# Optimization experiments

Measured on AMD Instinct MI355X. Metric: run time of the kernel, lower is better.

Reference implementation:

```python
import jax, jax.numpy as jnp
import numpy as np

ALPHA = 1.5      # entmax alpha (q parameter)
N_ITER = 50      # entmax-bisect iterations (entmax library default)
B, S, DM, H, HKV, HD = 1, 2048, 2048, 16, 4, 128
ROPE_THETA = 10000.0


def _entmax_p(x):
    """alpha-entmax along last axis via bisection on tau (matches entmax.EntmaxBisect)."""
    am1 = ALPHA - 1.0
    pw = 1.0 / am1
    X = x * am1
    d = x.shape[-1]
    max_val = jnp.max(X, axis=-1, keepdims=True)
    tau_lo = max_val - 1.0                      # _gp(1, alpha) = 1
    tau_hi = max_val - (1.0 / d) ** am1          # _gp(1/d, alpha)
    dm0 = tau_hi - tau_lo

    def body(i, carry):
        tau_lo, dm, tau_m = carry
        dm = dm * 0.5
        tau_m = tau_lo + dm
        p = jnp.maximum(X - tau_m, 0.0) ** pw
        f = jnp.sum(p, axis=-1, keepdims=True) - 1.0
        tau_lo = jnp.where(f >= 0, tau_m, tau_lo)
        return (tau_lo, dm, tau_m)

    tau_lo, dm, tau_m = jax.lax.fori_loop(0, N_ITER, body, (tau_lo, dm0, tau_lo))
    p = jnp.maximum(X - tau_m, 0.0) ** pw
    return p / jnp.sum(p, axis=-1, keepdims=True)  # ensure_sum_one


@jax.custom_vjp
def entmax_bisect(x):
    return _entmax_p(x)

def _emx_fwd(x):
    p = _entmax_p(x)
    return p, p

def _emx_bwd(p, g):
    # entmax library backward: gppr = p^(2-alpha) on support
    gppr = jnp.where(p > 0, p ** (2.0 - ALPHA), 0.0)
    dX = g * gppr
    q = jnp.sum(dX, axis=-1, keepdims=True) / jnp.sum(gppr, axis=-1, keepdims=True)
    return ((dX - q * gppr),)

entmax_bisect.defvjp(_emx_fwd, _emx_bwd)


def _rotate_half(x):
    x1, x2 = x[..., : HD // 2], x[..., HD // 2:]
    return jnp.concatenate([-x2, x1], axis=-1)


def setup_inputs() -> dict:
    key = jax.random.key(0)
    k1, k2, k3, k4, k5 = jax.random.split(key, 5)
    hidden_states = jax.random.normal(k1, (B, S, DM), dtype=jnp.float32)
    wq = jax.random.normal(k2, (H * HD, DM), dtype=jnp.float32) * 0.02
    wk = jax.random.normal(k3, (HKV * HD, DM), dtype=jnp.float32) * 0.02
    wv = jax.random.normal(k4, (HKV * HD, DM), dtype=jnp.float32) * 0.02
    wo = jax.random.normal(k5, (DM, H * HD), dtype=jnp.float32) * 0.02
    # real Llama RoPE position embeddings
    inv_freq = 1.0 / (ROPE_THETA ** (np.arange(0, HD, 2, dtype=np.float32) / HD))
    pos = np.arange(S, dtype=np.float32)
    freqs = pos[:, None] * inv_freq[None, :]          # [S, HD/2]
    emb = np.concatenate([freqs, freqs], axis=-1)     # [S, HD]
    cos = jnp.asarray(np.cos(emb))[None]              # [1, S, HD]
    sin = jnp.asarray(np.sin(emb))[None]
    return {"hidden_states": hidden_states, "cos": cos, "sin": sin,
            "wq": wq, "wk": wk, "wv": wv, "wo": wo}


def reference(hidden_states, cos, sin, wq, wk, wv, wo):
    b, s, _ = hidden_states.shape
    scaling = HD ** -0.5
    # QKV projections -> [B, H, S, HD]
    q = (hidden_states @ wq.T).reshape(b, s, H, HD).transpose(0, 2, 1, 3)
    k = (hidden_states @ wk.T).reshape(b, s, HKV, HD).transpose(0, 2, 1, 3)
    v = (hidden_states @ wv.T).reshape(b, s, HKV, HD).transpose(0, 2, 1, 3)
    # RoPE (cos/sin broadcast over head axis)
    c, sn = cos[:, None, :, :], sin[:, None, :, :]
    q = q * c + _rotate_half(q) * sn
    k = k * c + _rotate_half(k) * sn
    # GQA: repeat kv heads
    g = H // HKV
    k = jnp.repeat(k, g, axis=1)
    v = jnp.repeat(v, g, axis=1)
    scores = jnp.einsum('bhqd,bhkd->bhqk', q, k) * scaling
    causal = jnp.tril(jnp.ones((s, s), dtype=bool))
    scores = jnp.where(causal, scores, -jnp.inf)
    attn = entmax_bisect(scores)                      # [B, H, S, S]
    out = jnp.einsum('bhqk,bhkd->bhqd', attn, v)
    out = out.transpose(0, 2, 1, 3).reshape(b, s, H * HD)
    out = out @ wo.T
    return (out, attn)
```

## Files before the change

### kernel.cpp

```cpp
#include <hip/hip_runtime.h>

typedef __bf16 bf16;
typedef __bf16 bf16x4 __attribute__((ext_vector_type(4)));
typedef __bf16 bf16x8 __attribute__((ext_vector_type(8)));
typedef float f32x4 __attribute__((ext_vector_type(4)));
typedef float f32x2 __attribute__((ext_vector_type(2)));
typedef _Float16 f16x2 __attribute__((ext_vector_type(2)));

#define S 2048
#define DM 2048
#define HD 128
#define H 16
#define NQKV 3072
#define NEWTON_ITERS 12
#define BROW 556
#define MASKV -30000.0f

__device__ __forceinline__ void gl2lds16(const void* g, void* l) {
    __builtin_amdgcn_global_load_lds(
        (const __attribute__((address_space(1))) void*)g,
        (__attribute__((address_space(3))) void*)l, 16, 0, 0);
}

__device__ __forceinline__ void nt_store4(f32x4 v, float* p) {
    __builtin_nontemporal_store(v, (f32x4*)p);
}

template <int CTRL, int RM>
__device__ __forceinline__ float dpp_zero(float x) {
    return __builtin_bit_cast(float, __builtin_amdgcn_update_dpp(
        0, __builtin_bit_cast(int, x), CTRL, RM, 0xf, false));
}
template <int CTRL, int RM>
__device__ __forceinline__ float dpp_self(float x) {
    int xi = __builtin_bit_cast(int, x);
    return __builtin_bit_cast(float, __builtin_amdgcn_update_dpp(xi, xi, CTRL, RM, 0xf, false));
}
__device__ __forceinline__ float wave_bcast63(float x) {
    return __builtin_bit_cast(float, __builtin_amdgcn_readlane(__builtin_bit_cast(int, x), 63));
}
__device__ __forceinline__ float wave_sum(float x) {
    x += dpp_zero<0x111, 0xf>(x);
    x += dpp_zero<0x112, 0xf>(x);
    x += dpp_zero<0x114, 0xf>(x);
    x += dpp_zero<0x118, 0xf>(x);
    x += dpp_zero<0x142, 0xa>(x);
    x += dpp_zero<0x143, 0xc>(x);
    return wave_bcast63(x);
}
__device__ __forceinline__ float wave_fmax(float x) {
    x = fmaxf(x, dpp_self<0x111, 0xf>(x));
    x = fmaxf(x, dpp_self<0x112, 0xf>(x));
    x = fmaxf(x, dpp_self<0x114, 0xf>(x));
    x = fmaxf(x, dpp_self<0x118, 0xf>(x));
    x = fmaxf(x, dpp_self<0x142, 0xa>(x));
    x = fmaxf(x, dpp_self<0x143, 0xc>(x));
    return wave_bcast63(x);
}

__global__ void cvt_all(const float* __restrict__ hid, const float* __restrict__ wq,
                        const float* __restrict__ wk, const float* __restrict__ wv,
                        const float* __restrict__ wo, bf16* __restrict__ bh,
                        bf16* __restrict__ bqkv, bf16* __restrict__ bwo) {
    int i = blockIdx.x * blockDim.x + threadIdx.x;
    const float* src;
    bf16* dst;
    int off;
    if (i < 1048576) { src = hid; dst = bh; off = i; }
    else if (i < 2097152) { src = wq; dst = bqkv; off = i - 1048576; }
    else if (i < 2359296) { src = wk; dst = bqkv + 2048 * 2048; off = i - 2097152; }
    else if (i < 2621440) { src = wv; dst = bqkv + 2048 * 2048 + 512 * 2048; off = i - 2359296; }
    else { src = wo; dst = bwo; off = i - 2621440; }
    float4 f = ((const float4*)src)[off];
    bf16x4 o;
    o[0] = (bf16)f.x; o[1] = (bf16)f.y; o[2] = (bf16)f.z; o[3] = (bf16)f.w;
    ((bf16x4*)dst)[off] = o;
}

template <int BM, int BN>
__global__ __launch_bounds__(256) void gemm_bt(const bf16* __restrict__ A,
                                               const bf16* __restrict__ B,
                                               float* __restrict__ C, int Ndim, int K) {
    __shared__ bf16 As[BM * 32];
    __shared__ bf16 Bs[BN * 32];
    int m0 = blockIdx.x * BM, n0 = blockIdx.y * BN;
    int t = threadIdx.x;
    int l = t & 63, w = t >> 6;
    int lane16 = l & 15, quad = l >> 4;

    const bf16* Abase = A + (size_t)m0 * K;
    const bf16* Bbase = B + (size_t)n0 * K;

    constexpr int MI = BM / 32, NI = BN / 32;
    int wm = (w & 1) * (BM / 2), wn = (w >> 1) * (BN / 2);
    f32x4 acc[MI][NI];
#pragma unroll
    for (int i = 0; i < MI; i++)
#pragma unroll
        for (int j = 0; j < NI; j++) acc[i][j] = (f32x4){0.f, 0.f, 0.f, 0.f};

    constexpr int AG = BM * 4;
    constexpr int BG = BN * 4;

    for (int k0 = 0; k0 < K; k0 += 32) {
#pragma unroll
        for (int it = 0; it < AG / 256; it++) {
            int c = it * 256 + t;
            gl2lds16(Abase + (size_t)(c >> 2) * K + k0 + (c & 3) * 8, &As[(c - l) * 8]);
        }
#pragma unroll
        for (int it = 0; it < BG / 256; it++) {
            int c = it * 256 + t;
            gl2lds16(Bbase + (size_t)(c >> 2) * K + k0 + (c & 3) * 8, &Bs[(c - l) * 8]);
        }
        __syncthreads();
        bf16x8 af[MI], bfr[NI];
#pragma unroll
        for (int i = 0; i < MI; i++)
            af[i] = *(const bf16x8*)&As[(wm + i * 16 + lane16) * 32 + quad * 8];
#pragma unroll
        for (int j = 0; j < NI; j++)
            bfr[j] = *(const bf16x8*)&Bs[(wn + j * 16 + lane16) * 32 + quad * 8];
#pragma unroll
        for (int i = 0; i < MI; i++)
#pragma unroll
            for (int j = 0; j < NI; j++)
                acc[i][j] = __builtin_amdgcn_mfma_f32_16x16x32_bf16(af[i], bfr[j], acc[i][j], 0, 0, 0);
        __syncthreads();
    }
#pragma unroll
    for (int i = 0; i < MI; i++)
#pragma unroll
        for (int j = 0; j < NI; j++) {
            float* cp = C + (size_t)(m0 + wm + i * 16 + quad * 4) * Ndim + n0 + wn + j * 16 + lane16;
#pragma unroll
            for (int r = 0; r < 4; r++) cp[(size_t)r * Ndim] = acc[i][j][r];
        }
}

__global__ void rope_qk(const float* __restrict__ qkv, const float* __restrict__ cosb,
                        const float* __restrict__ sinb, bf16* __restrict__ qs,
                        bf16* __restrict__ kb) {
    int col = blockIdx.x * 256 + threadIdx.x;
    int s = blockIdx.y;
    const float* row = qkv + (size_t)s * NQKV;
    float v = row[col];
    if (col < DM) {
        int h = col >> 7, d = col & 127;
        float c = cosb[s * HD + d], sn = sinb[s * HD + d];
        float other = row[(h << 7) + ((d < 64) ? (d + 64) : (d - 64))];
        float rot = (d < 64) ? -other : other;
        float o = v * c + rot * sn;
        qs[((size_t)h * S + s) * HD + d] = (bf16)(o * 0.04419417382415922f);
    } else {
        int c2 = col - DM;
        int kv = c2 >> 7, d = c2 & 127;
        float c = cosb[s * HD + d], sn = sinb[s * HD + d];
        float other = row[DM + (kv << 7) + ((d < 64) ? (d + 64) : (d - 64))];
        float rot = (d < 64) ? -other : other;
        float o = v * c + rot * sn;
        kb[((size_t)kv * S + s) * HD + d] = (bf16)o;
    }
}

__global__ __launch_bounds__(256) void vtrans(const float* __restrict__ qkv, bf16* __restrict__ vT) {
    __shared__ bf16 tile[64][66];
    int s0 = blockIdx.x * 64, y0 = blockIdx.y * 64;
    int t = threadIdx.x;
    int ty = t & 63, tr = t >> 6;
#pragma unroll
    for (int i = 0; i < 16; i++) {
        int s = tr + i * 4;
        float v = qkv[(size_t)(s0 + s) * NQKV + 2560 + y0 + ty];
        tile[s][ty] = (bf16)v;
    }
    __syncthreads();
#pragma unroll
    for (int i = 0; i < 16; i++) {
        int y = tr + i * 4;
        vT[(size_t)(y0 + y) * S + s0 + ty] = tile[ty][y];
    }
}

template <int SEGS>
__device__ __forceinline__ void attn_body(const bf16* __restrict__ qs, const bf16* __restrict__ kb,
                                          const bf16* __restrict__ vT, float* __restrict__ attn,
                                          bf16* __restrict__ o, int r0, int h,
                                          float (&buf)[16][BROW]) {
    constexpr int NREG2 = SEGS * 4;
    int jlen = r0 + 16;
    int l = threadIdx.x & 63;
    int w = threadIdx.x >> 6;
    int lane16 = l & 15, quad = l >> 4;

    const bf16* qrow = qs + ((size_t)h * S + (r0 + lane16)) * HD + quad * 8;
    bf16x8 afrag[4];
#pragma unroll
    for (int kc = 0; kc < 4; kc++) afrag[kc] = *(const bf16x8*)(qrow + kc * 32);

    const bf16* kbase = kb + (size_t)(h >> 2) * S * HD;
    const bf16* vbase = vT + (size_t)(h >> 2) * HD * S;
    f16x2 xr[NREG2];

#pragma unroll
    for (int sgi = 0; sgi < SEGS; sgi++) {
        int j0 = sgi * 512;
        float (*sb)[BROW] = buf;
#pragma unroll
        for (int tt = 0; tt < 2; tt++) {
            int t = w + tt * 16;
            int jt = j0 + t * 16;
            if (jt < jlen) {
                f32x4 acc = {0.f, 0.f, 0.f, 0.f};
                const bf16* kp = kbase + (size_t)(jt + lane16) * HD + quad * 8;
#pragma unroll
                for (int kc = 0; kc < 4; kc++) {
                    bf16x8 b = *(const bf16x8*)(kp + kc * 32);
                    acc = __builtin_amdgcn_mfma_f32_16x16x32_bf16(afrag[kc], b, acc, 0, 0, 0);
                }
                if (jt + 15 > r0) {
                    int jj = jt + lane16;
#pragma unroll
                    for (int r = 0; r < 4; r++) {
                        int rowi = quad * 4 + r;
                        float v = acc[r];
                        if (jj > r0 + rowi) v = MASKV;
                        sb[rowi][t * 16 + lane16] = v;
                    }
                } else {
#pragma unroll
                    for (int r = 0; r < 4; r++) sb[quad * 4 + r][t * 16 + lane16] = acc[r];
                }
            }
        }
        __syncthreads();
#pragma unroll
        for (int part = 0; part < 2; part++) {
            float4 fq = *(const float4*)&sb[w][part * 256 + l * 4];
            f32x2 lo, hi;
            if (sgi == SEGS - 1) {
                int jb = j0 + part * 256 + l * 4;
                lo = (f32x2){(jb + 0 < jlen) ? fq.x : MASKV, (jb + 1 < jlen) ? fq.y : MASKV};
                hi = (f32x2){(jb + 2 < jlen) ? fq.z : MASKV, (jb + 3 < jlen) ? fq.w : MASKV};
            } else {
                lo = (f32x2){fq.x, fq.y};
                hi = (f32x2){fq.z, fq.w};
            }
            xr[sgi * 4 + part * 2 + 0] = __builtin_convertvector(lo, f16x2);
            xr[sgi * 4 + part * 2 + 1] = __builtin_convertvector(hi, f16x2);
        }
        __syncthreads();
    }

    const f32x2 z2 = {0.f, 0.f};
    float mx = MASKV;
#pragma unroll
    for (int c = 0; c < NREG2; c++) {
        f32x2 x0 = __builtin_convertvector(xr[c], f32x2);
        mx = fmaxf(mx, fmaxf(x0[0], x0[1]));
    }
    float m = wave_fmax(mx);

    float tau = m - 1.0f;
#pragma unroll 1
    for (int it = 0; it < NEWTON_ITERS; it++) {
        f32x2 tvi = {tau, tau};
        f32x2 fa = z2, fb = z2, ga = z2, gb = z2;
#pragma unroll
        for (int c = 0; c < NREG2; c += 2) {
            f32x2 x0 = __builtin_convertvector(xr[c], f32x2);
            f32x2 t0 = __builtin_elementwise_max(x0 - tvi, z2);
            fa += t0 * t0; ga += t0;
            f32x2 x1 = __builtin_convertvector(xr[c + 1], f32x2);
            f32x2 t1 = __builtin_elementwise_max(x1 - tvi, z2);
            fb += t1 * t1; gb += t1;
        }
        f32x2 fv = fa + fb, gv = ga + gb;
        float f = wave_sum(fv[0] + fv[1]);
        float g = wave_sum(gv[0] + gv[1]);
        tau += (f - 1.0f) / (2.0f * g + 1e-20f);
    }

    f32x2 tv = {tau, tau};
    float inv;
    {
        f32x2 sa = z2, sbv = z2;
#pragma unroll
        for (int c = 0; c < NREG2; c += 2) {
            f32x2 x0 = __builtin_convertvector(xr[c], f32x2);
            f32x2 t0 = __builtin_elementwise_max(x0 - tv, z2);
            sa += t0 * t0;
            f32x2 x1 = __builtin_convertvector(xr[c + 1], f32x2);
            f32x2 t1 = __builtin_elementwise_max(x1 - tv, z2);
            sbv += t1 * t1;
        }
        f32x2 sv = sa + sbv;
        float ssum = wave_sum(sv[0] + sv[1]);
        inv = 1.0f / ssum;
    }

    int jt_o = (w & 7) * 16;
    int kh = (w >> 3) * 256;
    f32x4 acc_o = {0.f, 0.f, 0.f, 0.f};
    f32x2 inv2 = {inv, inv};

#pragma unroll
    for (int sgi = 0; sgi < SEGS; sgi++) {
        int j0 = sgi * 512;
        bf16 (*pb)[BROW] = (bf16(*)[BROW])(&buf[0][0]) + (sgi & 1) * 16;
#pragma unroll
        for (int part = 0; part < 2; part++) {
            f32x2 xa = __builtin_convertvector(xr[sgi * 4 + part * 2 + 0], f32x2);
            f32x2 xb = __builtin_convertvector(xr[sgi * 4 + part * 2 + 1], f32x2);
            f32x2 ta = __builtin_elementwise_max(xa - tv, z2);
            f32x2 tb = __builtin_elementwise_max(xb - tv, z2);
            f32x2 pa = (ta * ta) * inv2;
            f32x2 pb2 = (tb * tb) * inv2;
            bf16x4 pbv;
            pbv[0] = (bf16)pa[0]; pbv[1] = (bf16)pa[1];
            pbv[2] = (bf16)pb2[0]; pbv[3] = (bf16)pb2[1];
            *(bf16x4*)&pb[w][part * 256 + l * 4] = pbv;
        }
        __syncthreads();
#pragma unroll
        for (int ks = 0; ks < 8; ks++) {
            int kk = kh + ks * 32;
            bf16x8 a = *(const bf16x8*)&pb[lane16][kk + quad * 8];
            bf16x8 b = *(const bf16x8*)(vbase + (size_t)(jt_o + lane16) * S + j0 + kk + quad * 8);
            acc_o = __builtin_amdgcn_mfma_f32_16x16x32_bf16(a, b, acc_o, 0, 0, 0);
        }
    }

    __syncthreads();
    if (w >= 8) {
#pragma unroll
        for (int r = 0; r < 4; r++) buf[w - 8][l * 4 + r] = acc_o[r];
    }
    __syncthreads();
    if (w < 8) {
        bf16* op = o + (size_t)(r0 + quad * 4) * DM + h * HD + jt_o + lane16;
#pragma unroll
        for (int r = 0; r < 4; r++) {
            float v = acc_o[r] + buf[w][l * 4 + r];
            op[(size_t)r * DM] = (bf16)v;
        }
    }

    float* arow = attn + ((size_t)h * S + (r0 + w)) * S;
#pragma unroll
    for (int sgi = 0; sgi < SEGS; sgi++) {
        int j0 = sgi * 512;
#pragma unroll
        for (int part = 0; part < 2; part++) {
            f32x2 xa = __builtin_convertvector(xr[sgi * 4 + part * 2 + 0], f32x2);
            f32x2 xb = __builtin_convertvector(xr[sgi * 4 + part * 2 + 1], f32x2);
            f32x2 ta = __builtin_elementwise_max(xa - tv, z2);
            f32x2 tb = __builtin_elementwise_max(xb - tv, z2);
            f32x2 pa = (ta * ta) * inv2;
            f32x2 pb2 = (tb * tb) * inv2;
            f32x4 pv = {pa[0], pa[1], pb2[0], pb2[1]};
            nt_store4(pv, &arow[j0 + part * 256 + l * 4]);
        }
    }
    f32x4 z4 = {0.f, 0.f, 0.f, 0.f};
    for (int j = SEGS * 512 + l * 4; j < S; j += 256) nt_store4(z4, &arow[j]);
}

__global__ __attribute__((amdgpu_flat_work_group_size(1024, 1024), amdgpu_waves_per_eu(8)))
void attn_av_all(const bf16* __restrict__ qs,
                 const bf16* __restrict__ kb,
                 const bf16* __restrict__ vT,
                 float* __restrict__ attn,
                 bf16* __restrict__ o) {
    __shared__ float buf[16][BROW];
    int b = blockIdx.x;
    int h = b & 15;
    int qh = b >> 4;
    attn_body<4>(qs, kb, vT, attn, o, (96 + qh) * 16, h, buf);
    __syncthreads();
    attn_body<3>(qs, kb, vT, attn, o, (64 + qh) * 16, h, buf);
    __syncthreads();
    attn_body<2>(qs, kb, vT, attn, o, (32 + qh) * 16, h, buf);
    __syncthreads();
    attn_body<1>(qs, kb, vT, attn, o, qh * 16, h, buf);
}

extern "C" void kernel_launch(void* const* d_in, const int* in_sizes, int n_in,
                              void* d_out, int out_size, void* d_ws, size_t ws_size,
                              hipStream_t stream) {
    const float* hidden = (const float*)d_in[0];
    const float* cosb   = (const float*)d_in[1];
    const float* sinb   = (const float*)d_in[2];
    const float* wq     = (const float*)d_in[3];
    const float* wk     = (const float*)d_in[4];
    const float* wv     = (const float*)d_in[5];
    const float* wo     = (const float*)d_in[6];
    char* ws = (char*)d_ws;
    bf16*  bf_hidden = (bf16*)(ws);
    bf16*  bf_wqkv   = (bf16*)(ws + 8388608);
    bf16*  bf_wo     = (bf16*)(ws + 20971520);
    float* qkv_raw   = (float*)(ws + 29360128);
    bf16*  qsb       = (bf16*)(ws + 54525952);
    bf16*  kbb       = (bf16*)(ws + 62914560);
    bf16*  vTb       = (bf16*)(ws + 65011712);
    float* out  = (float*)d_out;
    float* attn = out + 4194304;

    cvt_all<<<dim3(14336), 256, 0, stream>>>(hidden, wq, wk, wv, wo, bf_hidden, bf_wqkv, bf_wo);

    gemm_bt<64, 128><<<dim3(32, 24), 256, 0, stream>>>(bf_hidden, bf_wqkv, qkv_raw, NQKV, DM);

    rope_qk<<<dim3(10, S), 256, 0, stream>>>(qkv_raw, cosb, sinb, qsb, kbb);
    vtrans<<<dim3(32, 8), 256, 0, stream>>>(qkv_raw, vTb);

    attn_av_all<<<dim3(512), 1024, 0, stream>>>(qsb, kbb, vTb, attn, bf_hidden);

    gemm_bt<64, 128><<<dim3(32, 16), 256, 0, stream>>>(bf_hidden, bf_wo, out, DM, DM);
}
```

Measured before the change: 606.5 us.

## Double-buffer GEMM LDS tiles and drop waves_per_eu hint on attention kernel

The projection GEMM now keeps two LDS buffers for A and B tiles and issues the global-to-LDS loads for the next K step before running MFMAs on the current one, aiming to overlap memory latency with compute. One barrier per iteration is removed. The attention kernel loses its amdgpu_waves_per_eu(8) attribute, which relaxes the register limit and may change occupancy. The remaining edits are renames. Risk: the async global_load_lds prefetch may not be waited on correctly before the single barrier, and doubling LDS can reduce GEMM occupancy.

```diff
diff --git a/kernel.cpp b/kernel.cpp
--- a/kernel.cpp
+++ b/kernel.cpp
@@ -81,8 +81,8 @@
 __global__ __launch_bounds__(256) void gemm_bt(const bf16* __restrict__ A,
                                                const bf16* __restrict__ B,
                                                float* __restrict__ C, int Ndim, int K) {
-    __shared__ bf16 As[BM * 32];
-    __shared__ bf16 Bs[BN * 32];
+    __shared__ bf16 As[2][BM * 32];
+    __shared__ bf16 Bs[2][BN * 32];
     int m0 = blockIdx.x * BM, n0 = blockIdx.y * BN;
     int t = threadIdx.x;
     int l = t & 63, w = t >> 6;
@@ -102,31 +102,38 @@
     constexpr int AG = BM * 4;
     constexpr int BG = BN * 4;
 
-    for (int k0 = 0; k0 < K; k0 += 32) {
+    auto stage = [&](int sel, int k0) {
 #pragma unroll
         for (int it = 0; it < AG / 256; it++) {
             int c = it * 256 + t;
-            gl2lds16(Abase + (size_t)(c >> 2) * K + k0 + (c & 3) * 8, &As[(c - l) * 8]);
+            gl2lds16(Abase + (size_t)(c >> 2) * K + k0 + (c & 3) * 8, &As[sel][(c - l) * 8]);
         }
 #pragma unroll
         for (int it = 0; it < BG / 256; it++) {
             int c = it * 256 + t;
-            gl2lds16(Bbase + (size_t)(c >> 2) * K + k0 + (c & 3) * 8, &Bs[(c - l) * 8]);
-        }
-        __syncthreads();
+            gl2lds16(Bbase + (size_t)(c >> 2) * K + k0 + (c & 3) * 8, &Bs[sel][(c - l) * 8]);
+        }
+    };
+
+    stage(0, 0);
+    __syncthreads();
+    int cur = 0;
+    for (int k0 = 0; k0 < K; k0 += 32) {
+        if (k0 + 32 < K) stage(cur ^ 1, k0 + 32);
         bf16x8 af[MI], bfr[NI];
 #pragma unroll
         for (int i = 0; i < MI; i++)
-            af[i] = *(const bf16x8*)&As[(wm + i * 16 + lane16) * 32 + quad * 8];
+            af[i] = *(const bf16x8*)&As[cur][(wm + i * 16 + lane16) * 32 + quad * 8];
 #pragma unroll
         for (int j = 0; j < NI; j++)
-            bfr[j] = *(const bf16x8*)&Bs[(wn + j * 16 + lane16) * 32 + quad * 8];
+            bfr[j] = *(const bf16x8*)&Bs[cur][(wn + j * 16 + lane16) * 32 + quad * 8];
 #pragma unroll
         for (int i = 0; i < MI; i++)
 #pragma unroll
             for (int j = 0; j < NI; j++)
                 acc[i][j] = __builtin_amdgcn_mfma_f32_16x16x32_bf16(af[i], bfr[j], acc[i][j], 0, 0, 0);
         __syncthreads();
+        cur ^= 1;
     }
 #pragma unroll
     for (int i = 0; i < MI; i++)
@@ -187,7 +194,7 @@
                                           const bf16* __restrict__ vT, float* __restrict__ attn,
                                           bf16* __restrict__ o, int r0, int h,
                                           float (&buf)[16][BROW]) {
-    constexpr int NREG2 = SEGS * 4;
+    constexpr int NR = SEGS * 4;
     int jlen = r0 + 16;
     int l = threadIdx.x & 63;
     int w = threadIdx.x >> 6;
@@ -200,12 +207,11 @@
 
     const bf16* kbase = kb + (size_t)(h >> 2) * S * HD;
     const bf16* vbase = vT + (size_t)(h >> 2) * HD * S;
-    f16x2 xr[NREG2];
+    f16x2 xr[NR];
 
 #pragma unroll
     for (int sgi = 0; sgi < SEGS; sgi++) {
         int j0 = sgi * 512;
-        float (*sb)[BROW] = buf;
 #pragma unroll
         for (int tt = 0; tt < 2; tt++) {
             int t = w + tt * 16;
@@ -225,18 +231,18 @@
                         int rowi = quad * 4 + r;
                         float v = acc[r];
                         if (jj > r0 + rowi) v = MASKV;
-                        sb[rowi][t * 16 + lane16] = v;
+                        buf[rowi][t * 16 + lane16] = v;
                     }
                 } else {
 #pragma unroll
-                    for (int r = 0; r < 4; r++) sb[quad * 4 + r][t * 16 + lane16] = acc[r];
+                    for (int r = 0; r < 4; r++) buf[quad * 4 + r][t * 16 + lane16] = acc[r];
                 }
             }
         }
         __syncthreads();
 #pragma unroll
         for (int part = 0; part < 2; part++) {
-            float4 fq = *(const float4*)&sb[w][part * 256 + l * 4];
+            float4 fq = *(const float4*)&buf[w][part * 256 + l * 4];
             f32x2 lo, hi;
             if (sgi == SEGS - 1) {
                 int jb = j0 + part * 256 + l * 4;
@@ -255,7 +261,7 @@
     const f32x2 z2 = {0.f, 0.f};
     float mx = MASKV;
 #pragma unroll
-    for (int c = 0; c < NREG2; c++) {
+    for (int c = 0; c < NR; c++) {
         f32x2 x0 = __builtin_convertvector(xr[c], f32x2);
         mx = fmaxf(mx, fmaxf(x0[0], x0[1]));
     }
@@ -267,7 +273,7 @@
         f32x2 tvi = {tau, tau};
         f32x2 fa = z2, fb = z2, ga = z2, gb = z2;
 #pragma unroll
-        for (int c = 0; c < NREG2; c += 2) {
+        for (int c = 0; c < NR; c += 2) {
             f32x2 x0 = __builtin_convertvector(xr[c], f32x2);
             f32x2 t0 = __builtin_elementwise_max(x0 - tvi, z2);
             fa += t0 * t0; ga += t0;
@@ -286,7 +292,7 @@
     {
         f32x2 sa = z2, sbv = z2;
 #pragma unroll
-        for (int c = 0; c < NREG2; c += 2) {
+        for (int c = 0; c < NR; c += 2) {
             f32x2 x0 = __builtin_convertvector(xr[c], f32x2);
             f32x2 t0 = __builtin_elementwise_max(x0 - tv, z2);
             sa += t0 * t0;
@@ -366,7 +372,7 @@
     for (int j = SEGS * 512 + l * 4; j < S; j += 256) nt_store4(z4, &arow[j]);
 }
 
-__global__ __attribute__((amdgpu_flat_work_group_size(1024, 1024), amdgpu_waves_per_eu(8)))
+__global__ __attribute__((amdgpu_flat_work_group_size(1024, 1024)))
 void attn_av_all(const bf16* __restrict__ qs,
                  const bf16* __restrict__ kb,
                  const bf16* __restrict__ vT,
```

New measurement: 623.1 us. 1.03x slower.
